# Kernel optimization log

Measured on AMD Instinct MI355X. Metric: run time of the kernel, lower is better.

The kernel has to match this reference:

```python
import jax, jax.numpy as jnp
import numpy as np

WINDOW_SIZES = (1, 2, 3)
ALPHA = 0.2          # LeakyReLU negative slope
NEG = -9e15          # mask fill value from the torch code


def _xavier(key, shape, gain=np.sqrt(2.0)):
    fan_in, fan_out = shape[0], shape[1]
    std = gain * np.sqrt(2.0 / (fan_in + fan_out))
    return jax.random.normal(key, shape, jnp.float32) * std


def setup_inputs() -> dict:
    key = jax.random.key(0)
    k1, k2, k3, k4, k5 = jax.random.split(key, 5)
    T, B, D, F = 512, 64, 256, 256  # turns, batch, input_dim, output_dim (must match)
    return {
        "local_semantic_vectors": jax.random.normal(k1, (T, B, D), jnp.float32),
        "input_turns": jax.random.randint(k2, (B,), 0, T),  # turns[bt] <= T-1
        "W": _xavier(k3, (D, F)),
        "a1": _xavier(k4, (F, 1)),
        "a2": _xavier(k5, (F, 1)),
    }


def _window_mean(x, w):
    # x: [B, T, D] -> sliding-window mean over axis 1 (window w), zero-padded at end.
    B, T, D = x.shape
    xp = jnp.pad(x, ((0, 0), (0, w - 1), (0, 0)))
    acc = xp[:, :T]
    for j in range(1, w):  # w <= 3, tiny unrolled loop
        acc = acc + xp[:, j:j + T]
    return acc / w


def reference(local_semantic_vectors, input_turns, W, a1, a2):
    # local_semantic_vectors: [T, B, D] -> [B, T, D]
    x = jnp.swapaxes(local_semantic_vectors, 0, 1)
    B, T, D = x.shape
    t_idx = jnp.arange(T)

    num = jnp.zeros((B, W.shape[1]), jnp.float32)
    vws = jnp.zeros((B,), jnp.float32)  # number of window sizes with cnt > 0

    for w in WINDOW_SIZES:
        # number of valid windows per sample: t runs while w+t-1 <= turns
        cnt = jnp.maximum(input_turns - w + 2, 0)                  # [B]
        valid = t_idx[None, :] < cnt[:, None]                      # [B, T]

        # pooled window vectors, zero beyond cnt (max_turn padded to T;
        # padded rows are fully masked and dropped, so the result matches)
        pooled = jnp.where(valid[:, :, None], _window_mean(x, w), 0.0)  # [B, T, D]

        # GAT-style masked self-attention
        h = pooled @ W                                             # [B, T, F]
        f1 = h @ a1                                                # [B, T, 1]
        f2 = h @ a2                                                # [B, T, 1]
        e = jax.nn.leaky_relu(f1 + jnp.swapaxes(f2, 1, 2), ALPHA)  # [B, T, T]
        mask = valid[:, :, None] & valid[:, None, :]
        attn = jax.nn.softmax(jnp.where(mask, e, NEG), axis=-1)
        h_prime = attn @ h                                         # [B, T, F]

        # mean over the first cnt rows
        denom = jnp.maximum(cnt, 1).astype(jnp.float32)
        inter = (h_prime * valid[:, :, None]).sum(axis=1) / denom[:, None]  # [B, F]

        has = (cnt > 0).astype(jnp.float32)
        num = num + inter * has[:, None]
        vws = vws + has

    # cnt is non-increasing in w, so windows with cnt>0 are exactly the first vws;
    # vws >= 1 always (w=1 gives cnt = turns + 2 >= 2).
    return num / vws[:, None]
```

## Files before the change

### kernel.cpp

```cpp
#include <hip/hip_runtime.h>
#include <math.h>

#define T_DIM 512
#define B_DIM 64
#define D_DIM 256
#define F_DIM 256
#define ALPHA 0.2f
#define L2E 1.44269504089f
#define NEGL -1.0e38f

#define U_OFF 0
#define V_OFF 256
#define P_OFF 512
#define Q_OFF (P_OFF + T_DIM * B_DIM)
#define GG_OFF (Q_OFF + T_DIM * B_DIM)

__global__ __launch_bounds__(256) void g_uv(const float* __restrict__ W,
                                            const float* __restrict__ a1,
                                            const float* __restrict__ a2,
                                            float* __restrict__ ws) {
    int tid = threadIdx.x;
    int wave = tid >> 6, lane = tid & 63;
    int d = blockIdx.x * 4 + wave;
    float4 wv = ((const float4*)(W + (size_t)d * F_DIM))[lane];
    float4 a1v = ((const float4*)a1)[lane];
    float4 a2v = ((const float4*)a2)[lane];
    float p = wv.x * a1v.x + wv.y * a1v.y + wv.z * a1v.z + wv.w * a1v.w;
    float q = wv.x * a2v.x + wv.y * a2v.y + wv.z * a2v.z + wv.w * a2v.w;
    for (int off = 32; off > 0; off >>= 1) {
        p += __shfl_down(p, off);
        q += __shfl_down(q, off);
    }
    if (lane == 0) {
        ws[U_OFF + d] = p;
        ws[V_OFF + d] = q;
    }
}

__global__ __launch_bounds__(512) void g_pq(const float* __restrict__ x,
                                            const int* __restrict__ turns,
                                            float* __restrict__ ws) {
    __shared__ float su[D_DIM], sv[D_DIM];
    int tid = threadIdx.x;
    if (tid < 64) ((float4*)su)[tid] = ((const float4*)(ws + U_OFF))[tid];
    else if (tid < 128) ((float4*)sv)[tid - 64] = ((const float4*)(ws + V_OFF))[tid - 64];
    __syncthreads();
    int lane = tid & 63;
    int gw = blockIdx.x * 8 + (tid >> 6);
    int b = gw & 63;
    int tbase = gw >> 6;
    int tn = turns[b];
    float4 uv = ((const float4*)su)[lane];
    float4 vv = ((const float4*)sv)[lane];
    float4 xv[8];
#pragma unroll
    for (int k = 0; k < 8; ++k) {
        int t = tbase + k * 64;
        if (t <= tn)
            xv[k] = ((const float4*)x)[((size_t)t * B_DIM + b) * (D_DIM / 4) + lane];
    }
#pragma unroll
    for (int k = 0; k < 8; ++k) {
        int t = tbase + k * 64;
        if (t <= tn) {
            float pp = xv[k].x * uv.x + xv[k].y * uv.y + xv[k].z * uv.z + xv[k].w * uv.w;
            float qq = xv[k].x * vv.x + xv[k].y * vv.y + xv[k].z * vv.z + xv[k].w * vv.w;
            for (int off = 32; off > 0; off >>= 1) {
                pp += __shfl_down(pp, off);
                qq += __shfl_down(qq, off);
            }
            if (lane == 0) {
                ws[P_OFF + b * T_DIM + t] = pp;
                ws[Q_OFF + b * T_DIM + t] = qq;
            }
        }
    }
}

__global__ __launch_bounds__(512) void g_attn(const int* __restrict__ turns,
                                              float* __restrict__ ws,
                                              float* __restrict__ out) {
    int bi = blockIdx.x, tid = threadIdx.x;
    if (bi < 32) out[bi * 512 + tid] = 0.f;
    int b = bi / 3, w = bi % 3 + 1;
    int tn = turns[b];
    int cnt = tn - w + 2;
    if (cnt > T_DIM) cnt = T_DIM;
    float* GG = ws + GG_OFF + ((w - 1) * B_DIM + b) * T_DIM;
    if (cnt <= 0) {
        GG[tid] = 0.f;
        return;
    }
    __shared__ float sp[T_DIM], sq[T_DIM], f2L[T_DIM], red[8];
    __shared__ float2 fc[T_DIM];
    if (tid < 128) {
        ((float4*)sp)[tid] = ((const float4*)(ws + P_OFF + b * T_DIM))[tid];
        ((float4*)sq)[tid] = ((const float4*)(ws + Q_OFF + b * T_DIM))[tid];
    }
    __syncthreads();
    float scale = L2E / (float)w;
    int j = tid;
    float vj;
    if (j < cnt) {
        float a = sq[j];
        if (w > 1) a += sq[j + 1];
        if (w > 2) a += sq[j + 2];
        vj = a * scale;
    } else {
        vj = NEGL;
    }
    f2L[j] = vj;
    float m = vj;
    for (int off = 32; off > 0; off >>= 1) m = fmaxf(m, __shfl_down(m, off));
    if ((tid & 63) == 0) red[tid >> 6] = m;
    __syncthreads();
    float M = red[0];
#pragma unroll
    for (int i2 = 1; i2 < 8; ++i2) M = fmaxf(M, red[i2]);
    if (j < cnt) {
        float a = sp[j];
        if (w > 1) a += sp[j + 1];
        if (w > 2) a += sp[j + 2];
        float f1 = a * scale;
        float s0 = f1 + M;
        float mrow = fmaxf(s0, ALPHA * s0);
        float r = 0.f;
        for (int jj = 0; jj < cnt; ++jj) {
            float s = f1 + f2L[jj];
            s = fmaxf(s, ALPHA * s);
            r += __builtin_amdgcn_exp2f(s - mrow);
        }
        fc[j] = make_float2(f1, mrow + __builtin_amdgcn_logf(r));
    }
    __syncthreads();
    float acc = 0.f;
    if (j < cnt) {
        for (int i = 0; i < cnt; ++i) {
            float2 t2 = fc[i];
            float s = t2.x + vj;
            s = fmaxf(s, ALPHA * s);
            acc += __builtin_amdgcn_exp2f(s - t2.y);
        }
        acc /= (float)cnt;
    }
    GG[j] = (j < cnt) ? acc : 0.f;
}

__global__ __launch_bounds__(512) void g_zout(const float* __restrict__ x,
                                              const int* __restrict__ turns,
                                              const float* __restrict__ W,
                                              const float* __restrict__ ws,
                                              float* __restrict__ out) {
    int b = blockIdx.x >> 2;
    int chunk = blockIdx.x & 3;
    int tn = turns[b];
    int t0 = chunk * 128;
    if (t0 > tn) return;
    int tid = threadIdx.x;
    __shared__ float Cs[128];
    __shared__ float4 zp[512];
    __shared__ float Zs[D_DIM];
    __shared__ float ored[512];
    if (tid < 128) {
        int t = t0 + tid;
        const float* G1 = ws + GG_OFF + (0 * B_DIM + b) * T_DIM;
        const float* G2 = ws + GG_OFF + (1 * B_DIM + b) * T_DIM;
        const float* G3 = ws + GG_OFF + (2 * B_DIM + b) * T_DIM;
        float g2 = G2[t] + (t >= 1 ? G2[t - 1] : 0.f);
        float g3 = G3[t] + (t >= 1 ? G3[t - 1] : 0.f) + (t >= 2 ? G3[t - 2] : 0.f);
        float vws = 1.f + (tn >= 1 ? 1.f : 0.f) + (tn >= 2 ? 1.f : 0.f);
        Cs[tid] = (G1[t] + 0.5f * g2 + (1.0f / 3.0f) * g3) / vws;
    }
    __syncthreads();
    int wave = tid >> 6, lane = tid & 63;
    float4 z = make_float4(0.f, 0.f, 0.f, 0.f);
    {
        int tg = t0 + wave * 16;
        size_t base = ((size_t)tg * B_DIM + b) * (D_DIM / 4) + lane;
#pragma unroll 8
        for (int tt = 0; tt < 16; ++tt) {
            float c = Cs[wave * 16 + tt];
            float4 xv = ((const float4*)x)[base + (size_t)tt * (B_DIM * D_DIM / 4)];
            z.x += c * xv.x; z.y += c * xv.y; z.z += c * xv.z; z.w += c * xv.w;
        }
    }
    zp[tid] = z;
    __syncthreads();
    if (tid < 64) {
        float4 a = zp[tid];
#pragma unroll
        for (int k = 1; k < 8; ++k) {
            float4 bb = zp[k * 64 + tid];
            a.x += bb.x; a.y += bb.y; a.z += bb.z; a.w += bb.w;
        }
        ((float4*)Zs)[tid] = a;
    }
    __syncthreads();
    int f = tid & 255, dh = tid >> 8;
    float acc = 0.f;
#pragma unroll 8
    for (int dd = dh * 128; dd < dh * 128 + 128; ++dd)
        acc += Zs[dd] * W[(size_t)dd * F_DIM + f];
    ored[tid] = acc;
    __syncthreads();
    if (tid < 256)
        atomicAdd(&out[b * F_DIM + tid], ored[tid] + ored[tid + 256]);
}

extern "C" void kernel_launch(void* const* d_in, const int* in_sizes, int n_in,
                              void* d_out, int out_size, void* d_ws, size_t ws_size,
                              hipStream_t stream) {
    const float* x = (const float*)d_in[0];
    const int* turns = (const int*)d_in[1];
    const float* W = (const float*)d_in[2];
    const float* a1 = (const float*)d_in[3];
    const float* a2 = (const float*)d_in[4];
    float* out = (float*)d_out;
    float* ws = (float*)d_ws;

    g_uv<<<B_DIM, 256, 0, stream>>>(W, a1, a2, ws);
    g_pq<<<512, 512, 0, stream>>>(x, turns, ws);
    g_attn<<<B_DIM * 3, 512, 0, stream>>>(turns, ws, out);
    g_zout<<<B_DIM * 4, 512, 0, stream>>>(x, turns, W, ws, out);
}
```

Before: 55.37 us.

## Restructure pipeline: fuse front stages, split attention row sums across blocks

Merges the u/v and p/q projection kernels into one per-batch kernel that also computes per-window column maxima. The O(cnt^2) softmax row-sum pass is split into 12 blocks per batch, which accumulate partial sums through atomics. The column-sum pass is folded into the final z/out kernel, computed per 128-turn chunk. The aim is to spread the serial quadratic attention work over more blocks and cut a launch. In exchange, the front kernel runs only 64 blocks and recomputes W·a per block, and the final kernel duplicates the column work for halo entries.

```diff
diff --git a/kernel.cpp b/kernel.cpp
--- a/kernel.cpp
+++ b/kernel.cpp
@@ -9,174 +9,267 @@
 #define L2E 1.44269504089f
 #define NEGL -1.0e38f
 
-#define U_OFF 0
-#define V_OFF 256
-#define P_OFF 512
-#define Q_OFF (P_OFF + T_DIM * B_DIM)
-#define GG_OFF (Q_OFF + T_DIM * B_DIM)
-
-__global__ __launch_bounds__(256) void g_uv(const float* __restrict__ W,
-                                            const float* __restrict__ a1,
-                                            const float* __restrict__ a2,
-                                            float* __restrict__ ws) {
-    int tid = threadIdx.x;
+#define P_OFF 0
+#define Q_OFF (P_OFF + B_DIM * T_DIM)
+#define M_OFF (Q_OFF + B_DIM * T_DIM)
+#define R_OFF (M_OFF + 3 * B_DIM)
+
+__device__ __forceinline__ float dot4(float4 a, float4 b) {
+    return a.x * b.x + a.y * b.y + a.z * b.z + a.w * b.w;
+}
+
+__global__ __launch_bounds__(1024) void g_front(const float* __restrict__ x,
+                                                const int* __restrict__ turns,
+                                                const float* __restrict__ W,
+                                                const float* __restrict__ a1,
+                                                const float* __restrict__ a2,
+                                                float* __restrict__ ws,
+                                                float* __restrict__ out) {
+    int b = blockIdx.x, tid = threadIdx.x;
     int wave = tid >> 6, lane = tid & 63;
-    int d = blockIdx.x * 4 + wave;
-    float4 wv = ((const float4*)(W + (size_t)d * F_DIM))[lane];
-    float4 a1v = ((const float4*)a1)[lane];
-    float4 a2v = ((const float4*)a2)[lane];
-    float p = wv.x * a1v.x + wv.y * a1v.y + wv.z * a1v.z + wv.w * a1v.w;
-    float q = wv.x * a2v.x + wv.y * a2v.y + wv.z * a2v.z + wv.w * a2v.w;
-    for (int off = 32; off > 0; off >>= 1) {
-        p += __shfl_down(p, off);
-        q += __shfl_down(q, off);
-    }
-    if (lane == 0) {
-        ws[U_OFF + d] = p;
-        ws[V_OFF + d] = q;
-    }
-}
-
-__global__ __launch_bounds__(512) void g_pq(const float* __restrict__ x,
-                                            const int* __restrict__ turns,
-                                            float* __restrict__ ws) {
+    __shared__ float a1s[F_DIM], a2s[F_DIM];
     __shared__ float su[D_DIM], sv[D_DIM];
-    int tid = threadIdx.x;
-    if (tid < 64) ((float4*)su)[tid] = ((const float4*)(ws + U_OFF))[tid];
-    else if (tid < 128) ((float4*)sv)[tid - 64] = ((const float4*)(ws + V_OFF))[tid - 64];
-    __syncthreads();
-    int lane = tid & 63;
-    int gw = blockIdx.x * 8 + (tid >> 6);
-    int b = gw & 63;
-    int tbase = gw >> 6;
+    __shared__ float sp[T_DIM], sq[T_DIM];
+    __shared__ float red[3][8];
+
+    if (tid < 256) out[b * F_DIM + tid] = 0.f;
+    for (int k = tid; k < 3 * T_DIM; k += 1024)
+        ws[R_OFF + ((k >> 9) * B_DIM + b) * T_DIM + (k & 511)] = 0.f;
+    if (tid < 64) ((float4*)a1s)[tid] = ((const float4*)a1)[tid];
+    else if (tid < 128) ((float4*)a2s)[tid - 64] = ((const float4*)a2)[tid - 64];
+    __syncthreads();
+
+    {
+        float4 A = ((const float4*)a1s)[lane];
+        float4 Bv = ((const float4*)a2s)[lane];
+#pragma unroll 4
+        for (int i = 0; i < 16; ++i) {
+            int d = wave + 16 * i;
+            float4 wv = ((const float4*)(W + (size_t)d * F_DIM))[lane];
+            float p = dot4(wv, A), q = dot4(wv, Bv);
+            for (int off = 32; off > 0; off >>= 1) {
+                p += __shfl_down(p, off);
+                q += __shfl_down(q, off);
+            }
+            if (lane == 0) { su[d] = p; sv[d] = q; }
+        }
+    }
+    __syncthreads();
+
     int tn = turns[b];
-    float4 uv = ((const float4*)su)[lane];
-    float4 vv = ((const float4*)sv)[lane];
-    float4 xv[8];
+    {
+        float4 uu = ((const float4*)su)[lane];
+        float4 vv = ((const float4*)sv)[lane];
+#pragma unroll 4
+        for (int i = 0; i < 32; ++i) {
+            int t = wave + 16 * i;
+            if (t <= tn) {
+                float4 xv = ((const float4*)x)[((size_t)t * B_DIM + b) * (D_DIM / 4) + lane];
+                float pp = dot4(xv, uu), qq = dot4(xv, vv);
+                for (int off = 32; off > 0; off >>= 1) {
+                    pp += __shfl_down(pp, off);
+                    qq += __shfl_down(qq, off);
+                }
+                if (lane == 0) {
+                    sp[t] = pp; sq[t] = qq;
+                    ws[P_OFF + b * T_DIM + t] = pp;
+                    ws[Q_OFF + b * T_DIM + t] = qq;
+                }
+            }
+        }
+    }
+    __syncthreads();
+
+    if (tid < 512) {
+        int j = tid;
 #pragma unroll
-    for (int k = 0; k < 8; ++k) {
-        int t = tbase + k * 64;
-        if (t <= tn)
-            xv[k] = ((const float4*)x)[((size_t)t * B_DIM + b) * (D_DIM / 4) + lane];
-    }
+        for (int w = 1; w <= 3; ++w) {
+            int cnt = tn - w + 2;
+            if (cnt > T_DIM) cnt = T_DIM;
+            float v = NEGL;
+            if (j < cnt) {
+                float a = sq[j];
+                if (w > 1) a += sq[j + 1];
+                if (w > 2) a += sq[j + 2];
+                v = a * (L2E / (float)w);
+            }
+            float m = v;
+            for (int off = 32; off > 0; off >>= 1) m = fmaxf(m, __shfl_down(m, off));
+            if (lane == 0) red[w - 1][wave] = m;
+        }
+    }
+    __syncthreads();
+    if (tid < 3) {
+        float M = red[tid][0];
 #pragma unroll
-    for (int k = 0; k < 8; ++k) {
-        int t = tbase + k * 64;
-        if (t <= tn) {
-            float pp = xv[k].x * uv.x + xv[k].y * uv.y + xv[k].z * uv.z + xv[k].w * uv.w;
-            float qq = xv[k].x * vv.x + xv[k].y * vv.y + xv[k].z * vv.z + xv[k].w * vv.w;
-            for (int off = 32; off > 0; off >>= 1) {
-                pp += __shfl_down(pp, off);
-                qq += __shfl_down(qq, off);
-            }
-            if (lane == 0) {
-                ws[P_OFF + b * T_DIM + t] = pp;
-                ws[Q_OFF + b * T_DIM + t] = qq;
-            }
-        }
-    }
-}
-
-__global__ __launch_bounds__(512) void g_attn(const int* __restrict__ turns,
-                                              float* __restrict__ ws,
-                                              float* __restrict__ out) {
+        for (int k = 1; k < 8; ++k) M = fmaxf(M, red[tid][k]);
+        ws[M_OFF + tid * B_DIM + b] = M;
+    }
+}
+
+__global__ __launch_bounds__(512) void g_row(const int* __restrict__ turns,
+                                             float* __restrict__ ws) {
     int bi = blockIdx.x, tid = threadIdx.x;
-    if (bi < 32) out[bi * 512 + tid] = 0.f;
-    int b = bi / 3, w = bi % 3 + 1;
+    int b = bi / 12, rem = bi % 12;
+    int w = (rem >> 2) + 1, jc = rem & 3;
     int tn = turns[b];
     int cnt = tn - w + 2;
     if (cnt > T_DIM) cnt = T_DIM;
-    float* GG = ws + GG_OFF + ((w - 1) * B_DIM + b) * T_DIM;
-    if (cnt <= 0) {
-        GG[tid] = 0.f;
-        return;
-    }
-    __shared__ float sp[T_DIM], sq[T_DIM], f2L[T_DIM], red[8];
-    __shared__ float2 fc[T_DIM];
+    if (cnt <= 0) return;
+    int j0 = jc * 128;
+    if (j0 >= cnt) return;
+    __shared__ float sp[T_DIM], f2L[128];
+    if (tid < 128) ((float4*)sp)[tid] = ((const float4*)(ws + P_OFF + b * T_DIM))[tid];
     if (tid < 128) {
-        ((float4*)sp)[tid] = ((const float4*)(ws + P_OFF + b * T_DIM))[tid];
-        ((float4*)sq)[tid] = ((const float4*)(ws + Q_OFF + b * T_DIM))[tid];
-    }
-    __syncthreads();
-    float scale = L2E / (float)w;
-    int j = tid;
-    float vj;
-    if (j < cnt) {
-        float a = sq[j];
-        if (w > 1) a += sq[j + 1];
-        if (w > 2) a += sq[j + 2];
-        vj = a * scale;
-    } else {
-        vj = NEGL;
-    }
-    f2L[j] = vj;
-    float m = vj;
-    for (int off = 32; off > 0; off >>= 1) m = fmaxf(m, __shfl_down(m, off));
-    if ((tid & 63) == 0) red[tid >> 6] = m;
-    __syncthreads();
-    float M = red[0];
-#pragma unroll
-    for (int i2 = 1; i2 < 8; ++i2) M = fmaxf(M, red[i2]);
-    if (j < cnt) {
-        float a = sp[j];
-        if (w > 1) a += sp[j + 1];
-        if (w > 2) a += sp[j + 2];
-        float f1 = a * scale;
+        int j = j0 + tid;
+        float v = NEGL;
+        if (j < cnt) {
+            const float* Q = ws + Q_OFF + b * T_DIM;
+            float a = Q[j];
+            if (w > 1) a += Q[j + 1];
+            if (w > 2) a += Q[j + 2];
+            v = a * (L2E / (float)w);
+        }
+        f2L[tid] = v;
+    }
+    __syncthreads();
+    float M = ws[M_OFF + (w - 1) * B_DIM + b];
+    int i = tid;
+    if (i < cnt) {
+        float a = sp[i];
+        if (w > 1) a += sp[i + 1];
+        if (w > 2) a += sp[i + 2];
+        float f1 = a * (L2E / (float)w);
         float s0 = f1 + M;
         float mrow = fmaxf(s0, ALPHA * s0);
         float r = 0.f;
-        for (int jj = 0; jj < cnt; ++jj) {
-            float s = f1 + f2L[jj];
+        int n = min(128, cnt - j0);
+        for (int k = 0; k < n; ++k) {
+            float s = f1 + f2L[k];
             s = fmaxf(s, ALPHA * s);
             r += __builtin_amdgcn_exp2f(s - mrow);
         }
-        fc[j] = make_float2(f1, mrow + __builtin_amdgcn_logf(r));
-    }
-    __syncthreads();
-    float acc = 0.f;
-    if (j < cnt) {
-        for (int i = 0; i < cnt; ++i) {
-            float2 t2 = fc[i];
-            float s = t2.x + vj;
-            s = fmaxf(s, ALPHA * s);
-            acc += __builtin_amdgcn_exp2f(s - t2.y);
-        }
-        acc /= (float)cnt;
-    }
-    GG[j] = (j < cnt) ? acc : 0.f;
-}
-
-__global__ __launch_bounds__(512) void g_zout(const float* __restrict__ x,
-                                              const int* __restrict__ turns,
-                                              const float* __restrict__ W,
-                                              const float* __restrict__ ws,
-                                              float* __restrict__ out) {
-    int b = blockIdx.x >> 2;
-    int chunk = blockIdx.x & 3;
+        atomicAdd(&ws[R_OFF + ((w - 1) * B_DIM + b) * T_DIM + i], r);
+    }
+}
+
+__global__ __launch_bounds__(512) void g_colzout(const float* __restrict__ x,
+                                                 const int* __restrict__ turns,
+                                                 const float* __restrict__ W,
+                                                 const float* __restrict__ ws,
+                                                 float* __restrict__ out) {
+    int b = blockIdx.x >> 2, chunk = blockIdx.x & 3;
     int tn = turns[b];
     int t0 = chunk * 128;
     if (t0 > tn) return;
     int tid = threadIdx.x;
+    __shared__ float sp[T_DIM], sq[T_DIM];
+    __shared__ float fx[T_DIM], fy[T_DIM];
+    __shared__ float Gs[3][130];
+    __shared__ float partq[128][4];
+    __shared__ float part2[2][128];
     __shared__ float Cs[128];
     __shared__ float4 zp[512];
     __shared__ float Zs[D_DIM];
     __shared__ float ored[512];
+
     if (tid < 128) {
-        int t = t0 + tid;
-        const float* G1 = ws + GG_OFF + (0 * B_DIM + b) * T_DIM;
-        const float* G2 = ws + GG_OFF + (1 * B_DIM + b) * T_DIM;
-        const float* G3 = ws + GG_OFF + (2 * B_DIM + b) * T_DIM;
-        float g2 = G2[t] + (t >= 1 ? G2[t - 1] : 0.f);
-        float g3 = G3[t] + (t >= 1 ? G3[t - 1] : 0.f) + (t >= 2 ? G3[t - 2] : 0.f);
+        ((float4*)sp)[tid] = ((const float4*)(ws + P_OFF + b * T_DIM))[tid];
+        ((float4*)sq)[tid] = ((const float4*)(ws + Q_OFF + b * T_DIM))[tid];
+    }
+    __syncthreads();
+
+    for (int w = 1; w <= 3; ++w) {
+        int cnt = tn - w + 2;
+        if (cnt > T_DIM) cnt = T_DIM;
+        bool active = cnt > 0;
+        float scale = L2E / (float)w;
+        float Mw = active ? ws[M_OFF + (w - 1) * B_DIM + b] : 0.f;
+        if (active) {
+            int i = tid;
+            if (i < cnt) {
+                float a = sp[i];
+                if (w > 1) a += sp[i + 1];
+                if (w > 2) a += sp[i + 2];
+                float f1 = a * scale;
+                float s0 = f1 + Mw;
+                float mrow = fmaxf(s0, ALPHA * s0);
+                float ri = ws[R_OFF + ((w - 1) * B_DIM + b) * T_DIM + i];
+                fx[i] = f1;
+                fy[i] = mrow + __builtin_amdgcn_logf(ri);
+            }
+        } else if (tid < 130) {
+            Gs[w - 1][tid] = 0.f;
+        }
+        __syncthreads();
+        if (active) {
+            {
+                int jj = tid >> 2, q = tid & 3;
+                int j = t0 + jj;
+                float acc = 0.f;
+                if (j < cnt) {
+                    float a = sq[j];
+                    if (w > 1) a += sq[j + 1];
+                    if (w > 2) a += sq[j + 2];
+                    float f2j = a * scale;
+                    int i1 = min((q + 1) * 128, cnt);
+                    for (int i = q * 128; i < i1; ++i) {
+                        float s = fx[i] + f2j;
+                        s = fmaxf(s, ALPHA * s);
+                        acc += __builtin_amdgcn_exp2f(s - fy[i]);
+                    }
+                }
+                partq[jj][q] = acc;
+            }
+            if (tid < 256) {
+                int e = tid >> 7, q = tid & 127;
+                int j = t0 - 2 + e;
+                float acc = 0.f;
+                if (j >= 0 && j < cnt) {
+                    float a = sq[j];
+                    if (w > 1) a += sq[j + 1];
+                    if (w > 2) a += sq[j + 2];
+                    float f2j = a * scale;
+                    for (int i = q; i < cnt; i += 128) {
+                        float s = fx[i] + f2j;
+                        s = fmaxf(s, ALPHA * s);
+                        acc += __builtin_amdgcn_exp2f(s - fy[i]);
+                    }
+                }
+                part2[e][q] = acc;
+            }
+        }
+        __syncthreads();
+        if (active) {
+            float invc = 1.0f / (float)cnt;
+            if (tid < 128) {
+                int j = t0 + tid;
+                float s = partq[tid][0] + partq[tid][1] + partq[tid][2] + partq[tid][3];
+                Gs[w - 1][2 + tid] = (j < cnt) ? s * invc : 0.f;
+            } else if (tid < 130) {
+                int e = tid - 128;
+                int j = t0 - 2 + e;
+                float s = 0.f;
+                for (int k = 0; k < 128; ++k) s += part2[e][k];
+                Gs[w - 1][e] = (j >= 0 && j < cnt) ? s * invc : 0.f;
+            }
+        }
+        __syncthreads();
+    }
+
+    if (tid < 128) {
+        float g1 = Gs[0][2 + tid];
+        float g2 = Gs[1][2 + tid] + Gs[1][1 + tid];
+        float g3 = Gs[2][2 + tid] + Gs[2][1 + tid] + Gs[2][tid];
         float vws = 1.f + (tn >= 1 ? 1.f : 0.f) + (tn >= 2 ? 1.f : 0.f);
-        Cs[tid] = (G1[t] + 0.5f * g2 + (1.0f / 3.0f) * g3) / vws;
-    }
-    __syncthreads();
+        Cs[tid] = (g1 + 0.5f * g2 + (1.0f / 3.0f) * g3) / vws;
+    }
+    __syncthreads();
+
     int wave = tid >> 6, lane = tid & 63;
     float4 z = make_float4(0.f, 0.f, 0.f, 0.f);
     {
-        int tg = t0 + wave * 16;
-        size_t base = ((size_t)tg * B_DIM + b) * (D_DIM / 4) + lane;
+        size_t base = ((size_t)(t0 + wave * 16) * B_DIM + b) * (D_DIM / 4) + lane;
 #pragma unroll 8
         for (int tt = 0; tt < 16; ++tt) {
             float c = Cs[wave * 16 + tt];
@@ -218,8 +311,7 @@
     float* out = (float*)d_out;
     float* ws = (float*)d_ws;
 
-    g_uv<<<B_DIM, 256, 0, stream>>>(W, a1, a2, ws);
-    g_pq<<<512, 512, 0, stream>>>(x, turns, ws);
-    g_attn<<<B_DIM * 3, 512, 0, stream>>>(turns, ws, out);
-    g_zout<<<B_DIM * 4, 512, 0, stream>>>(x, turns, W, ws, out);
-}
+    g_front<<<B_DIM, 1024, 0, stream>>>(x, turns, W, a1, a2, ws, out);
+    g_row<<<B_DIM * 12, 512, 0, stream>>>(turns, ws);
+    g_colzout<<<B_DIM * 4, 512, 0, stream>>>(x, turns, W, ws, out);
+}
```

Result: slower. 79.71 us (+43.9%).

## Fuse uv, pq and attention kernels into one 1024-thread block per sample-window

Applied to the files above, without the earlier changes.

Merges the three kernels (W·a projection, per-turn p/q dot products, attention softmax) into a single kernel, with each block recomputing u/v from W and p/q from x for its sample. Both O(cnt²) loops are split across two halves of a 1024-thread block and combined through shared-memory partial sums. This removes two kernel launches and the global workspace round trip. The cost is redundant work: each of the three window blocks per sample recomputes the same u/v and p/q, re-reading W and that sample's x.

```diff
diff --git a/kernel.cpp b/kernel.cpp
--- a/kernel.cpp
+++ b/kernel.cpp
@@ -9,141 +9,163 @@
 #define L2E 1.44269504089f
 #define NEGL -1.0e38f
 
-#define U_OFF 0
-#define V_OFF 256
-#define P_OFF 512
-#define Q_OFF (P_OFF + T_DIM * B_DIM)
-#define GG_OFF (Q_OFF + T_DIM * B_DIM)
-
-__global__ __launch_bounds__(256) void g_uv(const float* __restrict__ W,
-                                            const float* __restrict__ a1,
-                                            const float* __restrict__ a2,
-                                            float* __restrict__ ws) {
-    int tid = threadIdx.x;
+#define GG_OFF 0
+
+__device__ __forceinline__ float dot4(float4 a, float4 b) {
+    return a.x * b.x + a.y * b.y + a.z * b.z + a.w * b.w;
+}
+
+__global__ __launch_bounds__(1024, 1) void g_attn_all(const float* __restrict__ x,
+                                                      const int* __restrict__ turns,
+                                                      const float* __restrict__ W,
+                                                      const float* __restrict__ a1,
+                                                      const float* __restrict__ a2,
+                                                      float* __restrict__ ws,
+                                                      float* __restrict__ out) {
+    int bi = blockIdx.x, tid = threadIdx.x;
     int wave = tid >> 6, lane = tid & 63;
-    int d = blockIdx.x * 4 + wave;
-    float4 wv = ((const float4*)(W + (size_t)d * F_DIM))[lane];
-    float4 a1v = ((const float4*)a1)[lane];
-    float4 a2v = ((const float4*)a2)[lane];
-    float p = wv.x * a1v.x + wv.y * a1v.y + wv.z * a1v.z + wv.w * a1v.w;
-    float q = wv.x * a2v.x + wv.y * a2v.y + wv.z * a2v.z + wv.w * a2v.w;
-    for (int off = 32; off > 0; off >>= 1) {
-        p += __shfl_down(p, off);
-        q += __shfl_down(q, off);
-    }
-    if (lane == 0) {
-        ws[U_OFF + d] = p;
-        ws[V_OFF + d] = q;
-    }
-}
-
-__global__ __launch_bounds__(512) void g_pq(const float* __restrict__ x,
-                                            const int* __restrict__ turns,
-                                            float* __restrict__ ws) {
-    __shared__ float su[D_DIM], sv[D_DIM];
-    int tid = threadIdx.x;
-    if (tid < 64) ((float4*)su)[tid] = ((const float4*)(ws + U_OFF))[tid];
-    else if (tid < 128) ((float4*)sv)[tid - 64] = ((const float4*)(ws + V_OFF))[tid - 64];
-    __syncthreads();
-    int lane = tid & 63;
-    int gw = blockIdx.x * 8 + (tid >> 6);
-    int b = gw & 63;
-    int tbase = gw >> 6;
-    int tn = turns[b];
-    float4 uv = ((const float4*)su)[lane];
-    float4 vv = ((const float4*)sv)[lane];
-    float4 xv[8];
-#pragma unroll
-    for (int k = 0; k < 8; ++k) {
-        int t = tbase + k * 64;
-        if (t <= tn)
-            xv[k] = ((const float4*)x)[((size_t)t * B_DIM + b) * (D_DIM / 4) + lane];
-    }
-#pragma unroll
-    for (int k = 0; k < 8; ++k) {
-        int t = tbase + k * 64;
-        if (t <= tn) {
-            float pp = xv[k].x * uv.x + xv[k].y * uv.y + xv[k].z * uv.z + xv[k].w * uv.w;
-            float qq = xv[k].x * vv.x + xv[k].y * vv.y + xv[k].z * vv.z + xv[k].w * vv.w;
-            for (int off = 32; off > 0; off >>= 1) {
-                pp += __shfl_down(pp, off);
-                qq += __shfl_down(qq, off);
-            }
-            if (lane == 0) {
-                ws[P_OFF + b * T_DIM + t] = pp;
-                ws[Q_OFF + b * T_DIM + t] = qq;
-            }
-        }
-    }
-}
-
-__global__ __launch_bounds__(512) void g_attn(const int* __restrict__ turns,
-                                              float* __restrict__ ws,
-                                              float* __restrict__ out) {
-    int bi = blockIdx.x, tid = threadIdx.x;
-    if (bi < 32) out[bi * 512 + tid] = 0.f;
+    if (bi < 32 && tid < 512) out[bi * 512 + tid] = 0.f;
     int b = bi / 3, w = bi % 3 + 1;
     int tn = turns[b];
     int cnt = tn - w + 2;
     if (cnt > T_DIM) cnt = T_DIM;
     float* GG = ws + GG_OFF + ((w - 1) * B_DIM + b) * T_DIM;
     if (cnt <= 0) {
-        GG[tid] = 0.f;
+        if (tid < 512) GG[tid] = 0.f;
         return;
     }
-    __shared__ float sp[T_DIM], sq[T_DIM], f2L[T_DIM], red[8];
-    __shared__ float2 fc[T_DIM];
-    if (tid < 128) {
-        ((float4*)sp)[tid] = ((const float4*)(ws + P_OFF + b * T_DIM))[tid];
-        ((float4*)sq)[tid] = ((const float4*)(ws + Q_OFF + b * T_DIM))[tid];
-    }
-    __syncthreads();
+
+    __shared__ float a1s[F_DIM], a2s[F_DIM], su[D_DIM], sv[D_DIM];
+    __shared__ float sp[T_DIM], sq[T_DIM], f2L[T_DIM], fx[T_DIM], fy[T_DIM];
+    __shared__ float part[2][T_DIM];
+    __shared__ float red[8];
+
+    if (tid < 64) ((float4*)a1s)[tid] = ((const float4*)a1)[tid];
+    else if (tid < 128) ((float4*)a2s)[tid - 64] = ((const float4*)a2)[tid - 64];
+    __syncthreads();
+
+    {
+        float4 A = ((const float4*)a1s)[lane];
+        float4 Bv = ((const float4*)a2s)[lane];
+        float4 wv[8];
+#pragma unroll
+        for (int c = 0; c < 2; ++c) {
+#pragma unroll
+            for (int j = 0; j < 8; ++j) {
+                int d = wave + 16 * (c * 8 + j);
+                wv[j] = ((const float4*)(W + (size_t)d * F_DIM))[lane];
+            }
+#pragma unroll
+            for (int j = 0; j < 8; ++j) {
+                int d = wave + 16 * (c * 8 + j);
+                float p = dot4(wv[j], A), q = dot4(wv[j], Bv);
+                for (int off = 32; off > 0; off >>= 1) {
+                    p += __shfl_down(p, off);
+                    q += __shfl_down(q, off);
+                }
+                if (lane == 0) { su[d] = p; sv[d] = q; }
+            }
+        }
+    }
+    __syncthreads();
+
+    {
+        float4 uu = ((const float4*)su)[lane];
+        float4 vv = ((const float4*)sv)[lane];
+        float4 xv[8];
+#pragma unroll
+        for (int c = 0; c < 4; ++c) {
+#pragma unroll
+            for (int j = 0; j < 8; ++j) {
+                int t = wave + 16 * (c * 8 + j);
+                if (t <= tn)
+                    xv[j] = ((const float4*)x)[((size_t)t * B_DIM + b) * (D_DIM / 4) + lane];
+            }
+#pragma unroll
+            for (int j = 0; j < 8; ++j) {
+                int t = wave + 16 * (c * 8 + j);
+                if (t <= tn) {
+                    float pp = dot4(xv[j], uu), qq = dot4(xv[j], vv);
+                    for (int off = 32; off > 0; off >>= 1) {
+                        pp += __shfl_down(pp, off);
+                        qq += __shfl_down(qq, off);
+                    }
+                    if (lane == 0) { sp[t] = pp; sq[t] = qq; }
+                }
+            }
+        }
+    }
+    __syncthreads();
+
     float scale = L2E / (float)w;
-    int j = tid;
-    float vj;
-    if (j < cnt) {
-        float a = sq[j];
-        if (w > 1) a += sq[j + 1];
-        if (w > 2) a += sq[j + 2];
-        vj = a * scale;
-    } else {
-        vj = NEGL;
-    }
-    f2L[j] = vj;
-    float m = vj;
-    for (int off = 32; off > 0; off >>= 1) m = fmaxf(m, __shfl_down(m, off));
-    if ((tid & 63) == 0) red[tid >> 6] = m;
+    if (tid < 512) {
+        int j = tid;
+        float v = NEGL;
+        if (j < cnt) {
+            float a = sq[j];
+            if (w > 1) a += sq[j + 1];
+            if (w > 2) a += sq[j + 2];
+            v = a * scale;
+        }
+        f2L[j] = v;
+        float m = v;
+        for (int off = 32; off > 0; off >>= 1) m = fmaxf(m, __shfl_down(m, off));
+        if (lane == 0) red[wave] = m;
+        if (j < cnt) {
+            float a = sp[j];
+            if (w > 1) a += sp[j + 1];
+            if (w > 2) a += sp[j + 2];
+            fx[j] = a * scale;
+        }
+    }
     __syncthreads();
     float M = red[0];
 #pragma unroll
-    for (int i2 = 1; i2 < 8; ++i2) M = fmaxf(M, red[i2]);
-    if (j < cnt) {
-        float a = sp[j];
-        if (w > 1) a += sp[j + 1];
-        if (w > 2) a += sp[j + 2];
-        float f1 = a * scale;
-        float s0 = f1 + M;
+    for (int k = 1; k < 8; ++k) M = fmaxf(M, red[k]);
+
+    {
+        int i = tid & 511, jh = tid >> 9;
+        float r = 0.f;
+        if (i < cnt) {
+            float f1 = fx[i];
+            float s0 = f1 + M;
+            float mrow = fmaxf(s0, ALPHA * s0);
+            int j0 = jh * 256, j1 = min(j0 + 256, cnt);
+            for (int j = j0; j < j1; ++j) {
+                float s = f1 + f2L[j];
+                s = fmaxf(s, ALPHA * s);
+                r += __builtin_amdgcn_exp2f(s - mrow);
+            }
+        }
+        part[jh][i] = r;
+    }
+    __syncthreads();
+    if (tid < 512 && tid < cnt) {
+        float s0 = fx[tid] + M;
         float mrow = fmaxf(s0, ALPHA * s0);
-        float r = 0.f;
-        for (int jj = 0; jj < cnt; ++jj) {
-            float s = f1 + f2L[jj];
-            s = fmaxf(s, ALPHA * s);
-            r += __builtin_amdgcn_exp2f(s - mrow);
-        }
-        fc[j] = make_float2(f1, mrow + __builtin_amdgcn_logf(r));
-    }
-    __syncthreads();
-    float acc = 0.f;
-    if (j < cnt) {
-        for (int i = 0; i < cnt; ++i) {
-            float2 t2 = fc[i];
-            float s = t2.x + vj;
-            s = fmaxf(s, ALPHA * s);
-            acc += __builtin_amdgcn_exp2f(s - t2.y);
-        }
-        acc /= (float)cnt;
-    }
-    GG[j] = (j < cnt) ? acc : 0.f;
+        fy[tid] = mrow + __builtin_amdgcn_logf(part[0][tid] + part[1][tid]);
+    }
+    __syncthreads();
+
+    {
+        int j = tid & 511, ih = tid >> 9;
+        float acc = 0.f;
+        if (j < cnt) {
+            float f2j = f2L[j];
+            int i0 = ih * 256, i1 = min(i0 + 256, cnt);
+            for (int i = i0; i < i1; ++i) {
+                float s = fx[i] + f2j;
+                s = fmaxf(s, ALPHA * s);
+                acc += __builtin_amdgcn_exp2f(s - fy[i]);
+            }
+        }
+        part[ih][j] = acc;
+    }
+    __syncthreads();
+    if (tid < 512) {
+        int j = tid;
+        GG[j] = (j < cnt) ? (part[0][j] + part[1][j]) / (float)cnt : 0.f;
+    }
 }
 
 __global__ __launch_bounds__(512) void g_zout(const float* __restrict__ x,
@@ -175,8 +197,7 @@
     int wave = tid >> 6, lane = tid & 63;
     float4 z = make_float4(0.f, 0.f, 0.f, 0.f);
     {
-        int tg = t0 + wave * 16;
-        size_t base = ((size_t)tg * B_DIM + b) * (D_DIM / 4) + lane;
+        size_t base = ((size_t)(t0 + wave * 16) * B_DIM + b) * (D_DIM / 4) + lane;
 #pragma unroll 8
         for (int tt = 0; tt < 16; ++tt) {
             float c = Cs[wave * 16 + tt];
@@ -218,8 +239,6 @@
     float* out = (float*)d_out;
     float* ws = (float*)d_ws;
 
-    g_uv<<<B_DIM, 256, 0, stream>>>(W, a1, a2, ws);
-    g_pq<<<512, 512, 0, stream>>>(x, turns, ws);
-    g_attn<<<B_DIM * 3, 512, 0, stream>>>(turns, ws, out);
+    g_attn_all<<<B_DIM * 3, 1024, 0, stream>>>(x, turns, W, a1, a2, ws, out);
     g_zout<<<B_DIM * 4, 512, 0, stream>>>(x, turns, W, ws, out);
 }
```

Measured after the change: 78.36 us. 41.5% more time.
